# Kernel tuning notes

Measured on AMD Instinct MI355X. Metric: run time of the kernel, lower is better.

## Reference

```python
import jax, jax.numpy as jnp
import numpy as np

CURVE = 1.0
TAU = 0.5
NB_RF = 64


def _mnorm(x):
    # Minkowski (Lorentz) inner product of x with itself, keepdims: [..., 1]
    return -x[..., :1] ** 2 + jnp.sum(x[..., 1:] ** 2, axis=-1, keepdims=True)


def _hyp_linear(x, W, b, c=CURVE):
    # HypLinear: linear map on space part, time recomputed to stay on hyperboloid.
    # x: [N, Din], W: [H, Din, Ds], b: [H, Ds] -> [H, N, Ds+1]
    space = jnp.einsum('nd,hds->hns', x, W) + b[:, None, :]
    time = jnp.sqrt(1.0 / c + jnp.sum(space ** 2, axis=-1, keepdims=True))
    return jnp.concatenate([time, space], axis=-1)


def _softmax_kernel(data, proj, tau=TAU, c=CURVE, eps=1e-8):
    # FAVOR+ style positive random-feature transform with hyperbolic time correction.
    t = data[..., :1]          # [H, N, 1] Lorentz time component
    s = data[..., 1:]          # [H, N, D-1] space components
    m = 1.0 / jnp.sqrt(jnp.float32(proj.shape[0]))
    wx = jnp.exp(jnp.einsum('hnd,dm->hnm', s, proj) / jnp.sqrt(jnp.float32(tau)))
    front = jnp.exp(((1.0 / c) / tau - t ** 2 / tau) / 2.0) * m + eps
    return wx * front          # [H, N, NB_RF]


def _kernelized(q, k, v, proj, c=CURVE):
    # O(N) linear attention: sum_n k'(n) v(n) then q' @ summary, plus Lorentz renorm.
    qp = _softmax_kernel(q, proj)
    kp = _softmax_kernel(k, proj)
    last = jnp.einsum('hnm,hnd->hmd', kp, v)      # [H, NB_RF, D]
    z = jnp.einsum('hnm,hmd->hnd', qp, last)      # [H, Nq, D]
    coeff = (1.0 / jnp.sqrt(c)) / jnp.sqrt(jnp.abs(_mnorm(z) + 1e-7))
    return z * coeff


def _mobius_add(a, b, c=CURVE):
    ab = jnp.sum(a * b, axis=-1, keepdims=True)
    a2 = jnp.sum(a * a, axis=-1, keepdims=True)
    b2 = jnp.sum(b * b, axis=-1, keepdims=True)
    num = (1.0 + 2.0 * c * ab + c * b2) * a + (1.0 - c * a2) * b
    den = 1.0 + 2.0 * c * ab + c * c * a2 * b2
    return num / (den + 1e-7)


def _hyper_agg(t, c=CURVE):
    # hyperbolic_mean with uniform 1/H weights: Lorentz centroid over heads.
    m = jnp.mean(t, axis=0)                       # [N, D]
    return jnp.sqrt(1.0 / c) * m / jnp.sqrt(jnp.abs(_mnorm(m)) + 1e-7)


def setup_inputs() -> dict:
    H, Din, Ds = 4, 257, 256
    Nu, Ni = 20000, 20000
    # Structured projection matrix: vstacked transposed orthogonal 64x64 blocks,
    # rows rescaled by chi-distributed norms (scaling=0 in the torch code).
    rng = np.random.default_rng(0)
    blocks = []
    for _ in range(Ds // NB_RF):
        q, _ = np.linalg.qr(rng.standard_normal((NB_RF, NB_RF)))
        blocks.append(q.T)
    final = np.vstack(blocks)                     # [Ds, NB_RF]
    mult = np.linalg.norm(rng.standard_normal((Ds, NB_RF)), axis=1)
    proj = jnp.asarray((mult[:, None] * final).astype(np.float32))
    key = jax.random.key(0)
    ks = jax.random.split(key, 5)
    u = jax.random.normal(ks[0], (Nu, Din), dtype=jnp.float32) * 0.3
    i = jax.random.normal(ks[1], (Ni, Din), dtype=jnp.float32) * 0.3
    Wk = jax.random.normal(ks[2], (H, Din, Ds), dtype=jnp.float32) * 0.01
    Wq = jax.random.normal(ks[3], (H, Din, Ds), dtype=jnp.float32) * 0.01
    Wv = jax.random.normal(ks[4], (H, Din, Ds), dtype=jnp.float32) * 0.01
    bk = jnp.zeros((H, Ds), dtype=jnp.float32)
    bq = jnp.zeros((H, Ds), dtype=jnp.float32)
    bv = jnp.zeros((H, Ds), dtype=jnp.float32)
    return {"u": u, "i": i, "Wk": Wk, "bk": bk, "Wq": Wq, "bq": bq,
            "Wv": Wv, "bv": bv, "proj": proj}


def reference(u, i, Wk, bk, Wq, bq, Wv, bv, proj):
    u_key = _hyp_linear(u, Wk, bk)
    i_key = _hyp_linear(i, Wk, bk)
    u_query = _hyp_linear(u, Wq, bq)
    i_query = _hyp_linear(i, Wq, bq)
    u_value = _hyp_linear(u, Wv, bv)
    i_value = _hyp_linear(i, Wv, bv)
    _u_value = _kernelized(u_query, i_key, i_value, proj)
    _i_value = _kernelized(i_query, u_key, u_value, proj)
    u_out = _mobius_add(u_value, _u_value)
    i_out = _mobius_add(i_value, _i_value)
    return _hyper_agg(u_out), _hyper_agg(i_out)
```

## Files before the change

### kernel.cpp

```cpp
#include <hip/hip_runtime.h>
#include <hip/hip_bf16.h>

#define HH 4
#define NR 20000
#define DIN 257
#define DS 256
#define MF 64
#define KP 288
#define VP 264
#define LTP 272
#define ZST 276
#define LKC 25

typedef __bf16 bf16;
typedef bf16 bf16x8 __attribute__((ext_vector_type(8)));
typedef bf16 bf16x4 __attribute__((ext_vector_type(4)));
typedef bf16 bf16x2 __attribute__((ext_vector_type(2)));
typedef float f32x4 __attribute__((ext_vector_type(4)));
typedef unsigned int u32x4 __attribute__((ext_vector_type(4)));

__global__ void cvt_x_kernel(const float* __restrict__ xA, const float* __restrict__ xB,
                             bf16* __restrict__ xbA, bf16* __restrict__ xbB) {
  const int n = blockIdx.x, k = threadIdx.x;
  const float* x = blockIdx.y ? xB : xA;
  bf16* xb = blockIdx.y ? xbB : xbA;
  bf16 v = (bf16)0.f;
  if (k < DIN) v = (bf16)x[(long)n * DIN + k];
  else if (k == DIN) v = (bf16)1.f;
  xb[(long)n * KP + k] = v;
}

__global__ void cvt_w_kernel(const float* __restrict__ Wq, const float* __restrict__ Wk,
                             const float* __restrict__ Wv, bf16* __restrict__ WbTq,
                             bf16* __restrict__ WbTk, bf16* __restrict__ WbTv) {
  const int which = blockIdx.y;
  const int h = blockIdx.x >> 8, n = blockIdx.x & 255, k = threadIdx.x;
  const float* W = which == 0 ? Wq : (which == 1 ? Wk : Wv);
  bf16* o = which == 0 ? WbTq : (which == 1 ? WbTk : WbTv);
  o[((long)h * 256 + n) * KP + k] =
      (k < DIN) ? (bf16)W[((long)h * DIN + k) * DS + n] : (bf16)0.f;
}

__global__ void cvt_wp_kernel(const float* __restrict__ Wq, const float* __restrict__ Wk,
                              const float* __restrict__ bq, const float* __restrict__ bk,
                              const float* __restrict__ proj, bf16* __restrict__ WpT) {
  const int k = blockIdx.x, h = blockIdx.y, which = blockIdx.z, m = threadIdx.x;
  const float* W = which ? Wk : Wq;
  const float* bb = which ? bk : bq;
  float acc = 0.f;
  if (k < DIN) {
    const float* wr = W + ((long)h * DIN + k) * DS;
#pragma unroll 8
    for (int d = 0; d < DS; d++) acc = fmaf(wr[d], proj[(long)d * MF + m], acc);
  } else if (k == DIN) {
    const float* br = bb + (long)h * DS;
#pragma unroll 8
    for (int d = 0; d < DS; d++) acc = fmaf(br[d], proj[(long)d * MF + m], acc);
  }
  WpT[(((long)which * HH + h) * MF + m) * KP + k] = (bf16)acc;
}

__device__ __forceinline__ void gl_lds16(const bf16* g, bf16* l) {
  __builtin_amdgcn_global_load_lds(
      (const __attribute__((address_space(1))) unsigned int*)g,
      (__attribute__((address_space(3))) unsigned int*)l, 16, 0, 0);
}

__global__ __launch_bounds__(256) void proj4_kernel(
    const bf16* __restrict__ xbA, const bf16* __restrict__ xbB,
    const bf16* __restrict__ WbTq, const bf16* __restrict__ WbTk,
    const bf16* __restrict__ WbTv, const bf16* __restrict__ WpT,
    const float* __restrict__ bq, const float* __restrict__ bk,
    const float* __restrict__ bv,
    bf16* __restrict__ voA, bf16* __restrict__ voB,
    bf16* __restrict__ qpA, bf16* __restrict__ kpA,
    bf16* __restrict__ qpB, bf16* __restrict__ kpB)
{
  __shared__ __align__(16) char smem[40960];
  bf16* Ab = (bf16*)smem;
  bf16* Bb = (bf16*)(smem + 8192);
  float (*rs)[4] = (float(*)[4])smem;
  float* frl = (float*)(smem + 2048);

  const int t = threadIdx.x;
  const int zh = blockIdx.x;
  const int h = zh & 3;
  const int z = zh >> 2;
  const int n0 = blockIdx.y * 64;
  const bf16* xb = (z == 1 || z >= 4) ? xbB : xbA;
  const bf16* WbT = (z < 2) ? WbTv : ((z == 2 || z == 4) ? WbTq : WbTk);
  const float* bsel = (z < 2) ? bv : ((z == 2 || z == 4) ? bq : bk);
  const int w = t >> 6, lane = t & 63;
  const int m16 = lane & 15, q = lane >> 4;
  const bf16* wbh = WbT + (long)h * 256 * KP;

  const int rsub = w * 16 + (lane >> 2);
  const int cb = (lane & 3) * 8;
  const bf16* gA = xb + (long)min(n0 + rsub, NR - 1) * KP + cb;
  const bf16* gB = wbh + (long)rsub * KP + cb;

  const int which = (z == 2 || z == 4) ? 0 : 1;
  const bf16* gWp = WpT + (((long)which * HH + h) * MF + (w * 16 + m16)) * KP + q * 8;

#define STAGE(buf, c)                                                        \
  do {                                                                       \
    const int _k0 = (c) * 32;                                                \
    gl_lds16(gA + _k0, Ab + (buf) * 2048 + w * 512);                         \
    _Pragma("unroll")                                                        \
    for (int e = 0; e < 4; e++)                                              \
      gl_lds16(gB + (long)e * 64 * KP + _k0,                                 \
               Bb + (buf) * 8192 + e * 2048 + w * 512);                      \
  } while (0)

  f32x4 acc[4][4] = {};
  f32x4 acc5[4] = {};
  STAGE(0, 0);

  for (int c = 0; c < 9; c++) {
    const int cur = c & 1;
    __syncthreads();
    if (c < 8) STAGE(1 - cur, c + 1);

    bf16x8 af[4], bfj[4];
#pragma unroll
    for (int i = 0; i < 4; i++)
      af[i] = *(const bf16x8*)(Ab + cur * 2048 + (i * 16 + m16) * 32 + q * 8);
#pragma unroll
    for (int j = 0; j < 4; j++)
      bfj[j] = *(const bf16x8*)(Bb + cur * 8192 + (w * 64 + j * 16 + m16) * 32 + q * 8);
#pragma unroll
    for (int i = 0; i < 4; i++)
#pragma unroll
      for (int j = 0; j < 4; j++)
        acc[i][j] = __builtin_amdgcn_mfma_f32_16x16x32_bf16(af[i], bfj[j], acc[i][j], 0, 0, 0);
    if (z >= 2) {
      const bf16x8 bf5 = *(const bf16x8*)(gWp + c * 32);
#pragma unroll
      for (int i = 0; i < 4; i++)
        acc5[i] = __builtin_amdgcn_mfma_f32_16x16x32_bf16(af[i], bf5, acc5[i], 0, 0, 0);
    }
  }
#undef STAGE

  __syncthreads();

  float bias[4];
#pragma unroll
  for (int j = 0; j < 4; j++) bias[j] = bsel[h * DS + w * 64 + j * 16 + m16];
#pragma unroll
  for (int i = 0; i < 4; i++)
#pragma unroll
    for (int r = 0; r < 4; r++) {
      float s = 0.f;
#pragma unroll
      for (int j = 0; j < 4; j++) {
        acc[i][j][r] += bias[j];
        s = fmaf(acc[i][j][r], acc[i][j][r], s);
      }
      for (int off = 1; off < 16; off <<= 1) s += __shfl_xor(s, off);
      if (m16 == 0) rs[i * 16 + q * 4 + r][w] = s;
    }
  __syncthreads();

  if (z < 2) {
    bf16* vout = z ? voB : voA;
    if (t < 64) {
      const float ss = rs[t][0] + rs[t][1] + rs[t][2] + rs[t][3];
      if (n0 + t < NR) vout[((long)h * NR + n0 + t) * VP] = (bf16)sqrtf(1.f + ss);
    }
#pragma unroll
    for (int i = 0; i < 4; i++) {
      const int row = i * 16 + q * 4;
#pragma unroll
      for (int r = 0; r < 4; r++) {
        const int rg = n0 + row + r;
        if (rg < NR) {
          bf16* vo = vout + ((long)h * NR + rg) * VP + 1 + w * 64 + m16;
          vo[0] = (bf16)acc[i][0][r]; vo[16] = (bf16)acc[i][1][r];
          vo[32] = (bf16)acc[i][2][r]; vo[48] = (bf16)acc[i][3][r];
        }
      }
    }
  } else {
    if (t < 64) {
      const float ss = rs[t][0] + rs[t][1] + rs[t][2] + rs[t][3];
      frl[t] = 0.125f * __expf(-ss) + 1e-8f;
    }
    __syncthreads();
    bf16* fout = (z == 2) ? qpA : (z == 3) ? kpA : (z == 4) ? qpB : kpB;
    const float SQ2 = 1.41421356237309515f;
#pragma unroll
    for (int i = 0; i < 4; i++) {
      const int row = i * 16 + q * 4;
#pragma unroll
      for (int r = 0; r < 4; r++) {
        const int rg = n0 + row + r;
        if (rg < NR) {
          const float frv = frl[row + r];
          fout[((long)h * NR + rg) * MF + w * 16 + m16] =
              (bf16)(__expf(SQ2 * acc5[i][r]) * frv);
        }
      }
    }
  }
}

__global__ __launch_bounds__(256) void last3_kernel(
    const bf16* __restrict__ vA, const bf16* __restrict__ fA,
    const bf16* __restrict__ vB, const bf16* __restrict__ fB,
    float* __restrict__ part)
{
  __shared__ unsigned int Va[64 * 17];
  __shared__ unsigned int Fa[64 * 17];
  const int t = threadIdx.x;
  const int dt = blockIdx.x, kc = blockIdx.y, z = blockIdx.z;
  const int side = z >> 2, h = z & 3;
  const bf16* v = side ? vB : vA;
  const bf16* f = side ? fB : fA;
  const int d0 = dt * 64;
  const int w = t >> 6, lane = t & 63;
  const int m16 = lane & 15, q = lane >> 4;
  const int np = t >> 4, xg = (t & 15) * 4;
  f32x4 acc[4] = {};

  auto loadv = [&](int c, bf16x4& a0, bf16x4& a1) {
    const int n0c = (kc * LKC + c) * 32;
    const bf16* s0 = v + ((long)h * NR + n0c + 2 * np) * VP + d0 + xg;
    const bf16* s1 = s0 + VP;
    if (d0 + xg + 3 < DIN) {
      a0 = *(const bf16x4*)s0;
      a1 = *(const bf16x4*)s1;
    } else {
#pragma unroll
      for (int e = 0; e < 4; e++) {
        const bool ok = (d0 + xg + e < DIN);
        a0[e] = ok ? s0[e] : (bf16)0.f;
        a1[e] = ok ? s1[e] : (bf16)0.f;
      }
    }
  };
  auto loadf = [&](int c, bf16x4& g0, bf16x4& g1) {
    const int n0c = (kc * LKC + c) * 32;
    const bf16* s0 = f + ((long)h * NR + n0c + 2 * np) * MF + xg;
    g0 = *(const bf16x4*)s0;
    g1 = *(const bf16x4*)(s0 + MF);
  };

  bf16x4 va0, va1, vf0, vf1;
  loadv(0, va0, va1);
  loadf(0, vf0, vf1);

  for (int c = 0; c < LKC; c++) {
#pragma unroll
    for (int e = 0; e < 4; e++) {
      bf16x2 pv; pv[0] = va0[e]; pv[1] = va1[e];
      Va[(xg + e) * 17 + np] = __builtin_bit_cast(unsigned int, pv);
      bf16x2 pf; pf[0] = vf0[e]; pf[1] = vf1[e];
      Fa[(xg + e) * 17 + np] = __builtin_bit_cast(unsigned int, pf);
    }
    bf16x4 na0 = va0, na1 = va1, nf0 = vf0, nf1 = vf1;
    if (c + 1 < LKC) { loadv(c + 1, na0, na1); loadf(c + 1, nf0, nf1); }
    __syncthreads();
    u32x4 bw;
#pragma unroll
    for (int c4 = 0; c4 < 4; c4++) bw[c4] = Fa[(w * 16 + m16) * 17 + q * 4 + c4];
    const bf16x8 bvv = __builtin_bit_cast(bf16x8, bw);
#pragma unroll
    for (int i = 0; i < 4; i++) {
      u32x4 aw;
#pragma unroll
      for (int c4 = 0; c4 < 4; c4++) aw[c4] = Va[(i * 16 + m16) * 17 + q * 4 + c4];
      acc[i] = __builtin_amdgcn_mfma_f32_16x16x32_bf16(
          __builtin_bit_cast(bf16x8, aw), bvv, acc[i], 0, 0, 0);
    }
    __syncthreads();
    va0 = na0; va1 = na1; vf0 = nf0; vf1 = nf1;
  }
  float* pp = part + ((long)(z * LKC + kc) * 5 + dt) * 4096;
#pragma unroll
  for (int i = 0; i < 4; i++)
#pragma unroll
    for (int r = 0; r < 4; r++)
      pp[(i * 16 + q * 4 + r) * 64 + w * 16 + m16] = acc[i][r];
}

__global__ void reduce_last4(const float* __restrict__ part,
                             bf16* __restrict__ hiU, bf16* __restrict__ loU,
                             bf16* __restrict__ hiI, bf16* __restrict__ loI) {
  const int d = blockIdx.x, zz = blockIdx.y, m = threadIdx.x;
  const int side = zz >> 2, h = zz & 3;
  const int dt = d >> 6, dl = d & 63;
  float s = 0.f;
#pragma unroll 5
  for (int kc = 0; kc < LKC; kc++)
    s += part[((long)(zz * LKC + kc) * 5 + dt) * 4096 + dl * 64 + m];
  bf16* hi = side ? hiI : hiU;
  bf16* lo = side ? loI : loU;
  const bf16 hv = (bf16)s;
  hi[((long)h * LTP + d) * MF + m] = hv;
  lo[((long)h * LTP + d) * MF + m] = (bf16)(s - (float)hv);
}

__global__ __launch_bounds__(256) void fuse3_kernel(
    const bf16* __restrict__ qpA, const bf16* __restrict__ vA,
    const bf16* __restrict__ hiA, const bf16* __restrict__ loA,
    const bf16* __restrict__ qpB, const bf16* __restrict__ vB,
    const bf16* __restrict__ hiB, const bf16* __restrict__ loB,
    float* __restrict__ out)
{
  __shared__ __align__(16) float zs[32 * ZST];

  const int side = blockIdx.y;
  const bf16* qp = side ? qpB : qpA;
  const bf16* v = side ? vB : vA;
  const bf16* hi = side ? hiB : hiA;
  const bf16* lo = side ? loB : loA;
  float* o = out + (long)side * NR * DIN;

  const int t = threadIdx.x;
  const int n0 = blockIdx.x * 32;
  const int w = t >> 6, lane = t & 63;
  const int m16 = lane & 15, q = lane >> 4;
  const int erow = t >> 3, ecol = (t & 7) * 4;
  const bool lead = ((t & 7) == 0);
  const int ntile = (w == 0) ? 5 : 4;

  f32x4 macc[8] = {};
  float macc256 = 0.f;

  for (int h = 0; h < HH; h++) {
    const bf16* vr = v + ((long)h * NR + n0 + erow) * VP;
    f32x4 vreg[8];
#pragma unroll
    for (int it = 0; it < 8; it++) {
      const bf16x4 vb = *(const bf16x4*)(vr + it * 32 + ecol);
#pragma unroll
      for (int c = 0; c < 4; c++) vreg[it][c] = (float)vb[c];
    }
    float v256 = lead ? (float)vr[256] : 0.f;

    bf16x8 af[2][2];
#pragma unroll
    for (int i = 0; i < 2; i++)
#pragma unroll
      for (int hf = 0; hf < 2; hf++)
        af[i][hf] = *(const bf16x8*)(qp + ((long)h * NR + n0 + i * 16 + m16) * MF + hf * 32 + q * 8);

    int d_cur = w * 16 + m16;
    bf16x8 bh0c, bh1c, bl0c, bl1c;
    {
      const bf16* ph = hi + ((long)h * LTP + d_cur) * MF + q * 8;
      const bf16* pl = lo + ((long)h * LTP + d_cur) * MF + q * 8;
      bh0c = *(const bf16x8*)ph; bh1c = *(const bf16x8*)(ph + 32);
      bl0c = *(const bf16x8*)pl; bl1c = *(const bf16x8*)(pl + 32);
    }
    for (int jt = 0; jt < ntile; jt++) {
      bf16x8 bh0n = bh0c, bh1n = bh1c, bl0n = bl0c, bl1n = bl1c;
      int d_nxt = d_cur;
      if (jt + 1 < ntile) {
        const int dtn = (jt + 1 < 4) ? (w + (jt + 1) * 4) : 16;
        d_nxt = dtn * 16 + m16;
        const bf16* ph = hi + ((long)h * LTP + d_nxt) * MF + q * 8;
        const bf16* pl = lo + ((long)h * LTP + d_nxt) * MF + q * 8;
        bh0n = *(const bf16x8*)ph; bh1n = *(const bf16x8*)(ph + 32);
        bl0n = *(const bf16x8*)pl; bl1n = *(const bf16x8*)(pl + 32);
      }
#pragma unroll
      for (int i = 0; i < 2; i++) {
        f32x4 a = {0.f, 0.f, 0.f, 0.f};
        a = __builtin_amdgcn_mfma_f32_16x16x32_bf16(af[i][1], bl1c, a, 0, 0, 0);
        a = __builtin_amdgcn_mfma_f32_16x16x32_bf16(af[i][0], bl0c, a, 0, 0, 0);
        a = __builtin_amdgcn_mfma_f32_16x16x32_bf16(af[i][1], bh1c, a, 0, 0, 0);
        a = __builtin_amdgcn_mfma_f32_16x16x32_bf16(af[i][0], bh0c, a, 0, 0, 0);
#pragma unroll
        for (int r = 0; r < 4; r++)
          zs[(i * 16 + q * 4 + r) * ZST + d_cur] = a[r];
      }
      bh0c = bh0n; bh1c = bh1n; bl0c = bl0n; bl1c = bl1n; d_cur = d_nxt;
    }
    __syncthreads();

    f32x4 zreg[8];
    float sz2 = 0.f, svz = 0.f, z0p = 0.f, v02p = 0.f;
#pragma unroll
    for (int it = 0; it < 8; it++) {
      zreg[it] = *(const f32x4*)&zs[erow * ZST + it * 32 + ecol];
#pragma unroll
      for (int c = 0; c < 4; c++) {
        sz2 = fmaf(zreg[it][c], zreg[it][c], sz2);
        svz = fmaf(vreg[it][c], zreg[it][c], svz);
      }
    }
    float z256 = 0.f;
    if (lead) {
      z256 = zs[erow * ZST + 256];
      sz2 = fmaf(z256, z256, sz2);
      svz = fmaf(v256, z256, svz);
      z0p = zreg[0][0];
      v02p = vreg[0][0] * vreg[0][0];
    }
#pragma unroll
    for (int off = 1; off < 8; off <<= 1) {
      sz2 += __shfl_xor(sz2, off);
      svz += __shfl_xor(svz, off);
      z0p += __shfl_xor(z0p, off);
      v02p += __shfl_xor(v02p, off);
    }
    const float a2 = 2.f * v02p - 1.f;
    const float mn = sz2 - 2.f * z0p * z0p;
    const float cf = 1.f / sqrtf(fabsf(mn + 1e-7f));
    const float ab = cf * svz;
    const float b2 = cf * cf * sz2;
    const float den = 1.f + 2.f * ab + a2 * b2;
    const float inv = 0.25f / (den + 1e-7f);
    const float sx = (1.f + 2.f * ab + b2) * inv;
    const float sy = (1.f - a2) * cf * inv;
#pragma unroll
    for (int it = 0; it < 8; it++)
#pragma unroll
      for (int c = 0; c < 4; c++)
        macc[it][c] = fmaf(sx, vreg[it][c], fmaf(sy, zreg[it][c], macc[it][c]));
    if (lead) macc256 = fmaf(sx, v256, fmaf(sy, z256, macc256));
    __syncthreads();
  }

  float sm2 = 0.f, m02p = 0.f;
#pragma unroll
  for (int it = 0; it < 8; it++)
#pragma unroll
    for (int c = 0; c < 4; c++) sm2 = fmaf(macc[it][c], macc[it][c], sm2);
  if (lead) {
    sm2 = fmaf(macc256, macc256, sm2);
    m02p = macc[0][0] * macc[0][0];
  }
#pragma unroll
  for (int off = 1; off < 8; off <<= 1) {
    sm2 += __shfl_xor(sm2, off);
    m02p += __shfl_xor(m02p, off);
  }
  const float fv = 1.f / sqrtf(fabsf(sm2 - 2.f * m02p) + 1e-7f);
  float* orow = o + (long)(n0 + erow) * DIN;
#pragma unroll
  for (int it = 0; it < 8; it++)
#pragma unroll
    for (int c = 0; c < 4; c++) orow[it * 32 + ecol + c] = macc[it][c] * fv;
  if (lead) orow[256] = macc256 * fv;
}

extern "C" void kernel_launch(void* const* d_in, const int* in_sizes, int n_in,
                              void* d_out, int out_size, void* d_ws, size_t ws_size,
                              hipStream_t stream) {
  const float* u    = (const float*)d_in[0];
  const float* ii   = (const float*)d_in[1];
  const float* Wk   = (const float*)d_in[2];
  const float* bk   = (const float*)d_in[3];
  const float* Wq   = (const float*)d_in[4];
  const float* bq   = (const float*)d_in[5];
  const float* Wv   = (const float*)d_in[6];
  const float* bv   = (const float*)d_in[7];
  const float* proj = (const float*)d_in[8];
  float* out = (float*)d_out;

  const long NVB = (long)HH * NR * VP;
  const long NF = (long)HH * NR * MF;
  const long NLT = (long)HH * LTP * MF;
  bf16* v_u = (bf16*)d_ws;
  bf16* v_i = v_u + NVB;
  bf16* qp_u = v_i + NVB;
  bf16* kp_u = qp_u + NF;
  bf16* qp_i = kp_u + NF;
  bf16* kp_i = qp_i + NF;
  bf16* ltHi_u = kp_i + NF;
  bf16* ltLo_u = ltHi_u + NLT;
  bf16* ltHi_i = ltLo_u + NLT;
  bf16* ltLo_i = ltHi_i + NLT;
  bf16* xb_u  = ltLo_i + NLT;
  bf16* xb_i  = xb_u + (long)NR * KP;
  bf16* WbTq  = xb_i + (long)NR * KP;
  bf16* WbTk  = WbTq + 4 * 256 * KP;
  bf16* WbTv  = WbTk + 4 * 256 * KP;
  bf16* WpT   = WbTv + 4 * 256 * KP;
  float* part = (float*)xb_u;

  cvt_x_kernel<<<dim3(NR, 2), KP, 0, stream>>>(u, ii, xb_u, xb_i);
  cvt_w_kernel<<<dim3(1024, 3), KP, 0, stream>>>(Wq, Wk, Wv, WbTq, WbTk, WbTv);
  cvt_wp_kernel<<<dim3(KP, HH, 2), 64, 0, stream>>>(Wq, Wk, bq, bk, proj, WpT);

  proj4_kernel<<<dim3(24, (NR + 63) / 64), 256, 0, stream>>>(
      xb_u, xb_i, WbTq, WbTk, WbTv, WpT, bq, bk, bv,
      v_u, v_i, qp_u, kp_u, qp_i, kp_i);

  last3_kernel<<<dim3(5, LKC, 8), 256, 0, stream>>>(v_i, kp_i, v_u, kp_u, part);
  reduce_last4<<<dim3(LTP, 8), 64, 0, stream>>>(part, ltHi_u, ltLo_u, ltHi_i, ltLo_i);

  fuse3_kernel<<<dim3(NR / 32, 2), 256, 0, stream>>>(
      qp_u, v_u, ltHi_u, ltLo_u, qp_i, v_i, ltHi_i, ltLo_i, out);
}
```

Measured before the change: 452.3 us.

## Double-buffer LDS in last3 kernel and drop register prefetch in z loop

The last3 reduction kernel now uses two LDS buffers. The next chunk is written into the alternate buffer after the MFMAs, so each iteration needs one barrier instead of two. Separately, the z-computation loop in the output kernel stops software-prefetching the next hi/lo tiles into registers and loads them directly each iteration. This lowers register pressure but exposes load latency. The extra LDS doubles shared memory use in last3, which may affect occupancy.

```diff
diff --git a/kernel.cpp b/kernel.cpp
--- a/kernel.cpp
+++ b/kernel.cpp
@@ -210,8 +210,8 @@
     const bf16* __restrict__ vB, const bf16* __restrict__ fB,
     float* __restrict__ part)
 {
-  __shared__ unsigned int Va[64 * 17];
-  __shared__ unsigned int Fa[64 * 17];
+  __shared__ unsigned int Va[2][64 * 17];
+  __shared__ unsigned int Fa[2][64 * 17];
   const int t = threadIdx.x;
   const int dt = blockIdx.x, kc = blockIdx.y, z = blockIdx.z;
   const int side = z >> 2, h = z & 3;
@@ -245,37 +245,43 @@
     g0 = *(const bf16x4*)s0;
     g1 = *(const bf16x4*)(s0 + MF);
   };
+  auto lwrite = [&](int buf, const bf16x4& a0, const bf16x4& a1,
+                    const bf16x4& g0, const bf16x4& g1) {
+#pragma unroll
+    for (int e = 0; e < 4; e++) {
+      bf16x2 pv; pv[0] = a0[e]; pv[1] = a1[e];
+      Va[buf][(xg + e) * 17 + np] = __builtin_bit_cast(unsigned int, pv);
+      bf16x2 pf; pf[0] = g0[e]; pf[1] = g1[e];
+      Fa[buf][(xg + e) * 17 + np] = __builtin_bit_cast(unsigned int, pf);
+    }
+  };
 
   bf16x4 va0, va1, vf0, vf1;
   loadv(0, va0, va1);
   loadf(0, vf0, vf1);
+  lwrite(0, va0, va1, vf0, vf1);
+  __syncthreads();
 
   for (int c = 0; c < LKC; c++) {
-#pragma unroll
-    for (int e = 0; e < 4; e++) {
-      bf16x2 pv; pv[0] = va0[e]; pv[1] = va1[e];
-      Va[(xg + e) * 17 + np] = __builtin_bit_cast(unsigned int, pv);
-      bf16x2 pf; pf[0] = vf0[e]; pf[1] = vf1[e];
-      Fa[(xg + e) * 17 + np] = __builtin_bit_cast(unsigned int, pf);
-    }
-    bf16x4 na0 = va0, na1 = va1, nf0 = vf0, nf1 = vf1;
-    if (c + 1 < LKC) { loadv(c + 1, na0, na1); loadf(c + 1, nf0, nf1); }
-    __syncthreads();
+    const int cur = c & 1;
+    if (c + 1 < LKC) { loadv(c + 1, va0, va1); loadf(c + 1, vf0, vf1); }
+
     u32x4 bw;
 #pragma unroll
-    for (int c4 = 0; c4 < 4; c4++) bw[c4] = Fa[(w * 16 + m16) * 17 + q * 4 + c4];
+    for (int c4 = 0; c4 < 4; c4++) bw[c4] = Fa[cur][(w * 16 + m16) * 17 + q * 4 + c4];
     const bf16x8 bvv = __builtin_bit_cast(bf16x8, bw);
 #pragma unroll
     for (int i = 0; i < 4; i++) {
       u32x4 aw;
 #pragma unroll
-      for (int c4 = 0; c4 < 4; c4++) aw[c4] = Va[(i * 16 + m16) * 17 + q * 4 + c4];
+      for (int c4 = 0; c4 < 4; c4++) aw[c4] = Va[cur][(i * 16 + m16) * 17 + q * 4 + c4];
       acc[i] = __builtin_amdgcn_mfma_f32_16x16x32_bf16(
           __builtin_bit_cast(bf16x8, aw), bvv, acc[i], 0, 0, 0);
     }
+    if (c + 1 < LKC) lwrite(1 - cur, va0, va1, vf0, vf1);
     __syncthreads();
-    va0 = na0; va1 = na1; vf0 = nf0; vf1 = nf1;
-  }
+  }
+
   float* pp = part + ((long)(z * LKC + kc) * 5 + dt) * 4096;
 #pragma unroll
   for (int i = 0; i < 4; i++)
@@ -346,37 +352,24 @@
       for (int hf = 0; hf < 2; hf++)
         af[i][hf] = *(const bf16x8*)(qp + ((long)h * NR + n0 + i * 16 + m16) * MF + hf * 32 + q * 8);
 
-    int d_cur = w * 16 + m16;
-    bf16x8 bh0c, bh1c, bl0c, bl1c;
-    {
-      const bf16* ph = hi + ((long)h * LTP + d_cur) * MF + q * 8;
-      const bf16* pl = lo + ((long)h * LTP + d_cur) * MF + q * 8;
-      bh0c = *(const bf16x8*)ph; bh1c = *(const bf16x8*)(ph + 32);
-      bl0c = *(const bf16x8*)pl; bl1c = *(const bf16x8*)(pl + 32);
-    }
     for (int jt = 0; jt < ntile; jt++) {
-      bf16x8 bh0n = bh0c, bh1n = bh1c, bl0n = bl0c, bl1n = bl1c;
-      int d_nxt = d_cur;
-      if (jt + 1 < ntile) {
-        const int dtn = (jt + 1 < 4) ? (w + (jt + 1) * 4) : 16;
-        d_nxt = dtn * 16 + m16;
-        const bf16* ph = hi + ((long)h * LTP + d_nxt) * MF + q * 8;
-        const bf16* pl = lo + ((long)h * LTP + d_nxt) * MF + q * 8;
-        bh0n = *(const bf16x8*)ph; bh1n = *(const bf16x8*)(ph + 32);
-        bl0n = *(const bf16x8*)pl; bl1n = *(const bf16x8*)(pl + 32);
-      }
+      const int dt = (jt < 4) ? (w + jt * 4) : 16;
+      const int d = dt * 16 + m16;
+      const bf16* ph = hi + ((long)h * LTP + d) * MF + q * 8;
+      const bf16* pl = lo + ((long)h * LTP + d) * MF + q * 8;
+      const bf16x8 bh0 = *(const bf16x8*)ph, bh1 = *(const bf16x8*)(ph + 32);
+      const bf16x8 bl0 = *(const bf16x8*)pl, bl1 = *(const bf16x8*)(pl + 32);
 #pragma unroll
       for (int i = 0; i < 2; i++) {
         f32x4 a = {0.f, 0.f, 0.f, 0.f};
-        a = __builtin_amdgcn_mfma_f32_16x16x32_bf16(af[i][1], bl1c, a, 0, 0, 0);
-        a = __builtin_amdgcn_mfma_f32_16x16x32_bf16(af[i][0], bl0c, a, 0, 0, 0);
-        a = __builtin_amdgcn_mfma_f32_16x16x32_bf16(af[i][1], bh1c, a, 0, 0, 0);
-        a = __builtin_amdgcn_mfma_f32_16x16x32_bf16(af[i][0], bh0c, a, 0, 0, 0);
+        a = __builtin_amdgcn_mfma_f32_16x16x32_bf16(af[i][1], bl1, a, 0, 0, 0);
+        a = __builtin_amdgcn_mfma_f32_16x16x32_bf16(af[i][0], bl0, a, 0, 0, 0);
+        a = __builtin_amdgcn_mfma_f32_16x16x32_bf16(af[i][1], bh1, a, 0, 0, 0);
+        a = __builtin_amdgcn_mfma_f32_16x16x32_bf16(af[i][0], bh0, a, 0, 0, 0);
 #pragma unroll
         for (int r = 0; r < 4; r++)
-          zs[(i * 16 + q * 4 + r) * ZST + d_cur] = a[r];
-      }
-      bh0c = bh0n; bh1c = bh1n; bl0c = bl0n; bl1c = bl1n; d_cur = d_nxt;
+          zs[(i * 16 + q * 4 + r) * ZST + d] = a[r];
+      }
     }
     __syncthreads();
 
```

Result: no change. 443.7 us (-1.9%).
